# Kernel optimization log

Hardware: AMD Instinct MI355X
Metric: run time of the kernel (lower is better)

Reference implementation:

```python
import jax, jax.numpy as jnp
import numpy as np

N, L, C = 2, 1024, 256
H, E, CL, LAYERS = 64, 16, 64, 4


def setup_inputs() -> dict:
    key = jax.random.key(0)
    ks = jax.random.split(key, 12)
    s = 0.05
    return {
        "x": jax.random.normal(ks[0], (N, L, C), jnp.float32),
        "Wq": jax.random.normal(ks[1], (H * E, C), jnp.float32) * s,
        "bq": jax.random.normal(ks[2], (H * E,), jnp.float32) * s,
        "Wk": jax.random.normal(ks[3], (H * E, C), jnp.float32) * s,
        "bk": jax.random.normal(ks[4], (H * E,), jnp.float32) * s,
        "Wv": jax.random.normal(ks[5], (H, C), jnp.float32) * s,
        "bv": jax.random.normal(ks[6], (H,), jnp.float32) * s,
        "PE": jax.random.uniform(ks[7], (CL, H, E), jnp.float32),
        "fc_w": jax.random.normal(ks[8], (LAYERS, H, H), jnp.float32) * s,
        "fc_b": jax.random.normal(ks[9], (LAYERS, H), jnp.float32) * s,
        "Wout": jax.random.normal(ks[10], (3, H), jnp.float32) * s,
        "bout": jax.random.normal(ks[11], (3,), jnp.float32) * s,
    }


def reference(x, Wq, bq, Wk, bk, Wv, bv, PE, fc_w, fc_b, Wout, bout):
    n, l, c = x.shape
    cl, h, e_dim = PE.shape
    q = (x @ Wq.T + bq).reshape(n, l, h, e_dim)   # (N,L,H,E)
    k = (x @ Wk.T + bk).reshape(n, l, h, e_dim)   # (N,L,H,E)
    v = x @ Wv.T + bv                             # (N,L,H)
    # sliding-window offsets: row i gathers positions i..i+cl-1
    off = jnp.arange(l - cl)[:, None] + jnp.arange(cl)[None, :]  # (L-cl, cl)
    q_mid = q[:, cl // 2: l - cl // 2]            # (N,L-cl,H,E) center queries
    k_win = k[:, off]                             # (N,L-cl,cl,H,E) gathered keys
    # e_{h,id} = q.k + q.PE  (distributed instead of adding PE to k_win)
    e = (jnp.einsum('nlhe,nldhe->nldh', q_mid, k_win)
         + jnp.einsum('nlhe,dhe->nldh', q_mid, PE))
    a = jax.nn.softmax(e, axis=2)                 # softmax over window offset d
    v_win = v[:, off]                             # (N,L-cl,cl,H)
    out = jnp.einsum('nldh,nldh->nlh', a, v_win)  # weighted sum over d
    out = jax.nn.relu(out)
    for i in range(fc_w.shape[0]):                # 1x1 Conv1d stack == per-pos linear
        out = jax.nn.relu(jnp.einsum('nlh,oh->nlo', out, fc_w[i]) + fc_b[i])
    out = jnp.einsum('nlh,oh->nlo', out, Wout) + bout  # (N,L-cl,3)
    return out
```

## Files before the change

kernel.cpp:

```cpp
#include <hip/hip_runtime.h>


typedef __attribute__((ext_vector_type(8))) __bf16 bf16x8;
typedef __attribute__((ext_vector_type(8))) short short8;
typedef __attribute__((ext_vector_type(16))) float f32x16;

__device__ inline unsigned short bf16_rne(float x) {
    unsigned u = __builtin_bit_cast(unsigned, x);
    unsigned r = u + 0x7fffu + ((u >> 16) & 1u);
    return (unsigned short)(r >> 16);
}
__device__ inline float bf16_f(unsigned short h) {
    return __builtin_bit_cast(float, (unsigned)h << 16);
}

__global__ __launch_bounds__(256) void convert_split(
    const float* __restrict__ X,
    const float* __restrict__ Wq, const float* __restrict__ Wk, const float* __restrict__ Wv,
    unsigned short* __restrict__ XhG, unsigned short* __restrict__ XlG,
    unsigned short* __restrict__ WhG, unsigned short* __restrict__ WlG)
{
    const int g = blockIdx.x * 256 + threadIdx.x;
    const int NX = 131072;
    const int NW = 135168;
    if (g >= NX + NW) return;

    float4 v;
    unsigned short *dh, *dl;
    int off;
    if (g < NX) {
        off = g * 4;
        v = *reinterpret_cast<const float4*>(&X[off]);
        dh = XhG; dl = XlG;
    } else {
        off = (g - NX) * 4;
        const int row = off >> 8, col = off & 255;
        const float* s;
        if (row < 1024)      s = &Wq[row * 256 + col];
        else if (row < 2048) s = &Wk[(row - 1024) * 256 + col];
        else                 s = &Wv[(row - 2048) * 256 + col];
        v = *reinterpret_cast<const float4*>(s);
        dh = WhG; dl = WlG;
    }
    unsigned short h0 = bf16_rne(v.x), h1 = bf16_rne(v.y), h2 = bf16_rne(v.z), h3 = bf16_rne(v.w);
    unsigned short l0 = bf16_rne(v.x - bf16_f(h0));
    unsigned short l1 = bf16_rne(v.y - bf16_f(h1));
    unsigned short l2 = bf16_rne(v.z - bf16_f(h2));
    unsigned short l3 = bf16_rne(v.w - bf16_f(h3));
    ushort4 hv = make_ushort4(h0, h1, h2, h3);
    ushort4 lv = make_ushort4(l0, l1, l2, l3);
    *reinterpret_cast<ushort4*>(&dh[off]) = hv;
    *reinterpret_cast<ushort4*>(&dl[off]) = lv;
}

__device__ __forceinline__ bf16x8 ldsfrag2(const unsigned short* lds, int base, int row, int so) {
    return __builtin_bit_cast(bf16x8, *reinterpret_cast<const short8*>(
        lds + base + row * 64 + (((so ^ (row & 7)) & 7) << 3)));
}

__global__ __launch_bounds__(256, 3) void qkv_mfma(
    const unsigned short* __restrict__ XhG, const unsigned short* __restrict__ XlG,
    const unsigned short* __restrict__ WhG, const unsigned short* __restrict__ WlG,
    const float* __restrict__ bq, const float* __restrict__ bk, const float* __restrict__ bv,
    float* __restrict__ qT, float* __restrict__ kT, float* __restrict__ vT)
{
    __shared__ unsigned short lds[24576];

    const int tid  = threadIdx.x;
    const int lane = tid & 63;
    const int wid  = tid >> 6;
    const int wm   = wid >> 1;
    const int wn   = wid & 1;

    const int job = blockIdx.x;
    int m0, o0;
    if (job < 512) { m0 = (job & 31) * 64; o0 = (job >> 5) * 128; }
    else           { m0 = (job - 512) * 64; o0 = 2048; }

    f32x16 acc[2];
    #pragma unroll
    for (int j = 0; j < 2; ++j)
        acc[j] = f32x16{0.f,0.f,0.f,0.f,0.f,0.f,0.f,0.f,0.f,0.f,0.f,0.f,0.f,0.f,0.f,0.f};

    const int r8 = lane >> 3;
    const int ss = (lane & 7) ^ r8;

    const int arow = wm * 32 + (lane & 31);
    const int kh   = lane >> 5;

    for (int k0 = 0; k0 < 256; k0 += 64) {
        #pragma unroll
        for (int j = 0; j < 12; ++j) {
            const int c = wid * 12 + j;
            const unsigned short* gsrc;
            if (c < 8)       gsrc = &XhG[(m0 + (c << 3) + r8) * 256 + k0 + (ss << 3)];
            else if (c < 16) gsrc = &XlG[(m0 + ((c - 8) << 3) + r8) * 256 + k0 + (ss << 3)];
            else if (c < 32) gsrc = &WhG[(o0 + ((c - 16) << 3) + r8) * 256 + k0 + (ss << 3)];
            else             gsrc = &WlG[(o0 + ((c - 32) << 3) + r8) * 256 + k0 + (ss << 3)];
            char* lbase = (char*)lds + (c << 10);
            __builtin_amdgcn_global_load_lds(
                (const __attribute__((address_space(1))) void*)gsrc,
                (__attribute__((address_space(3))) void*)lbase, 16, 0, 0);
        }
        __syncthreads();

        #pragma unroll
        for (int kk = 0; kk < 64; kk += 16) {
            const int so = (kk >> 3) + kh;
            bf16x8 aH = ldsfrag2(lds, 0,     arow, so);
            bf16x8 aL = ldsfrag2(lds, 4096,  arow, so);
            #pragma unroll
            for (int ot = 0; ot < 2; ++ot) {
                const int brow = wn * 64 + ot * 32 + (lane & 31);
                bf16x8 bH = ldsfrag2(lds, 8192,  brow, so);
                bf16x8 bL = ldsfrag2(lds, 16384, brow, so);
                acc[ot] = __builtin_amdgcn_mfma_f32_32x32x16_bf16(aH, bH, acc[ot], 0, 0, 0);
                acc[ot] = __builtin_amdgcn_mfma_f32_32x32x16_bf16(aH, bL, acc[ot], 0, 0, 0);
                acc[ot] = __builtin_amdgcn_mfma_f32_32x32x16_bf16(aL, bH, acc[ot], 0, 0, 0);
            }
        }
        __syncthreads();
    }

    const int dcol = lane & 31;
    const int rbase4 = 4 * (lane >> 5);
    const int mode = (o0 < 1024) ? 0 : (o0 < 2048 ? 1 : 2);

    if (mode < 2) {
        float* __restrict__ T = mode ? kT : qT;
        const float* __restrict__ bias = mode ? bk : bq;
        const int ob = mode * 1024;
        #pragma unroll
        for (int ot = 0; ot < 2; ++ot) {
            const int o = o0 + wn * 64 + ot * 32 + dcol;
            const int h = (o >> 4) & 63;
            const int e = o & 15;
            const float bval = bias[o - ob];
            #pragma unroll
            for (int r = 0; r < 16; ++r) {
                const int mrow = (r & 3) + 8 * (r >> 2) + rbase4;
                const int m = m0 + wm * 32 + mrow;
                const int n = m >> 10, l = m & 1023;
                T[((n * 64 + h) * 1024 + l) * 16 + e] = acc[ot][r] + bval;
            }
        }
    } else if (wn == 0) {
        #pragma unroll
        for (int ot = 0; ot < 2; ++ot) {
            const int hV = ot * 32 + dcol;
            const float bval = bv[hV];
            #pragma unroll
            for (int r = 0; r < 16; ++r) {
                const int mrow = (r & 3) + 8 * (r >> 2) + rbase4;
                const int m = m0 + wm * 32 + mrow;
                const int n = m >> 10, l = m & 1023;
                vT[(n * 64 + hV) * 1024 + l] = acc[ot][r] + bval;
            }
        }
    }
}

__global__ __launch_bounds__(256) void attn_kernel(
    const float* __restrict__ qT, const float* __restrict__ kT,
    const float* __restrict__ vT, const float* __restrict__ PE,
    float* __restrict__ attT)
{
    __shared__ float2 kc[8 * 322];
    __shared__ float pe_lds[64 * 16];
    __shared__ float v_lds[320];

    const int tid  = threadIdx.x;
    const int lane = tid & 63;
    const int w    = tid >> 6;
    const int xb = blockIdx.x;
    const int h  = blockIdx.y;
    const int n  = blockIdx.z;
    const int l0 = xb * 256;

    const int nrows = min(319, 1024 - l0);
    const float4* kb4 = reinterpret_cast<const float4*>(kT + ((size_t)(n * 64 + h) * 1024 + l0) * 16);
    for (int u = tid; u < nrows * 4; u += 256) {
        const int row = u >> 2, f = u & 3;
        const float4 g = kb4[u];
        kc[(2 * f + 0) * 322 + row] = make_float2(g.x, g.y);
        kc[(2 * f + 1) * 322 + row] = make_float2(g.z, g.w);
    }
    {
        const int d = tid >> 2, f = tid & 3;
        *reinterpret_cast<float4*>(&pe_lds[d * 16 + f * 4]) =
            *reinterpret_cast<const float4*>(&PE[(d * 64 + h) * 16 + f * 4]);
    }
    const float* vbase = vT + (size_t)(n * 64 + h) * 1024 + l0;
    for (int u = tid; u < nrows; u += 256) v_lds[u] = vbase[u];

    const int lout = l0 + w * 64 + lane;
    const bool active = lout < 960;
    const int lq = active ? lout : 959;
    float4 q0, q1, q2, q3;
    {
        const float4* qb = reinterpret_cast<const float4*>(
            qT + ((size_t)(n * 64 + h) * 1024 + lq + 32) * 16);
        q0 = qb[0]; q1 = qb[1]; q2 = qb[2]; q3 = qb[3];
    }
    __syncthreads();

    const int rbase = w * 64 + lane;
    float den = 0.f, pv = 0.f;
    #pragma unroll 2
    for (int d = 0; d < 64; ++d) {
        const int r = rbase + d;
        const float2 c0 = kc[0 * 322 + r], c1 = kc[1 * 322 + r];
        const float2 c2 = kc[2 * 322 + r], c3 = kc[3 * 322 + r];
        const float2 c4 = kc[4 * 322 + r], c5 = kc[5 * 322 + r];
        const float2 c6 = kc[6 * 322 + r], c7 = kc[7 * 322 + r];
        const float4* pr = reinterpret_cast<const float4*>(&pe_lds[d * 16]);
        const float4 p0 = pr[0], p1 = pr[1], p2 = pr[2], p3 = pr[3];
        float s0 = (c0.x + p0.x) * q0.x + (c0.y + p0.y) * q0.y
                 + (c1.x + p0.z) * q0.z + (c1.y + p0.w) * q0.w;
        float s1 = (c2.x + p1.x) * q1.x + (c2.y + p1.y) * q1.y
                 + (c3.x + p1.z) * q1.z + (c3.y + p1.w) * q1.w;
        float s2 = (c4.x + p2.x) * q2.x + (c4.y + p2.y) * q2.y
                 + (c5.x + p2.z) * q2.z + (c5.y + p2.w) * q2.w;
        float s3 = (c6.x + p3.x) * q3.x + (c6.y + p3.y) * q3.y
                 + (c7.x + p3.z) * q3.z + (c7.y + p3.w) * q3.w;
        const float s = (s0 + s1) + (s2 + s3);
        const float p = __expf(s - 16.f);
        den += p;
        pv += p * v_lds[r];
    }
    if (active)
        attT[(size_t)(n * 64 + h) * 960 + lout] = fmaxf(pv / den, 0.f);
}

__global__ __launch_bounds__(512) void fc_kernel(
    const float* __restrict__ attT,
    const float* __restrict__ fc_w, const float* __restrict__ fc_b,
    const float* __restrict__ Wout, const float* __restrict__ bout,
    float* __restrict__ out)
{
    __shared__ float w_lds[64 * 68];
    __shared__ float wo_lds[3 * 64];
    __shared__ float bufA[16 * 68];
    __shared__ float bufB[16 * 68];

    const int tid = threadIdx.x;
    const int o  = tid & 63;
    const int rr = tid >> 6;
    const int blk = blockIdx.x;
    const int n  = blk / 60;
    const int l0 = (blk - n * 60) * 16;
    const int R0 = n * 960 + l0;

    for (int idx = tid; idx < 192; idx += 512) wo_lds[idx] = Wout[idx];
    for (int idx = tid; idx < 1024; idx += 512) {
        const int hh = idx >> 4, r = idx & 15;
        bufA[r * 68 + hh] = attT[(size_t)(n * 64 + hh) * 960 + l0 + r];
    }

    float* cur = bufA;
    float* nxt = bufB;

    for (int layer = 0; layer < 4; ++layer) {
        __syncthreads();
        const float4* wsrc = reinterpret_cast<const float4*>(fc_w + layer * 4096);
        for (int u = tid; u < 1024; u += 512) {
            const int oo = u >> 4, f = u & 15;
            *reinterpret_cast<float4*>(&w_lds[oo * 68 + f * 4]) = wsrc[u];
        }
        __syncthreads();
        const float bias = fc_b[layer * 64 + o];
        const float4* wr = reinterpret_cast<const float4*>(&w_lds[o * 68]);
        #pragma unroll
        for (int rb = 0; rb < 2; ++rb) {
            const int r = rr + rb * 8;
            float acc = bias;
            const float4* cr = reinterpret_cast<const float4*>(&cur[r * 68]);
            #pragma unroll
            for (int t = 0; t < 16; ++t) {
                const float4 c = cr[t], wv = wr[t];
                acc += c.x * wv.x + c.y * wv.y + c.z * wv.z + c.w * wv.w;
            }
            nxt[r * 68 + o] = fmaxf(acc, 0.f);
        }
        float* tmp = cur; cur = nxt; nxt = tmp;
    }
    __syncthreads();

    if (o < 3) {
        #pragma unroll
        for (int rb = 0; rb < 2; ++rb) {
            const int r = rr + rb * 8;
            float acc = bout[o];
            #pragma unroll
            for (int hh = 0; hh < 64; ++hh)
                acc += cur[r * 68 + hh] * wo_lds[o * 64 + hh];
            out[(R0 + r) * 3 + o] = acc;
        }
    }
}

extern "C" void kernel_launch(void* const* d_in, const int* in_sizes, int n_in,
                              void* d_out, int out_size, void* d_ws, size_t ws_size,
                              hipStream_t stream) {
    const float* x    = (const float*)d_in[0];
    const float* Wq   = (const float*)d_in[1];
    const float* bq   = (const float*)d_in[2];
    const float* Wk   = (const float*)d_in[3];
    const float* bk   = (const float*)d_in[4];
    const float* Wv   = (const float*)d_in[5];
    const float* bv   = (const float*)d_in[6];
    const float* PE   = (const float*)d_in[7];
    const float* fc_w = (const float*)d_in[8];
    const float* fc_b = (const float*)d_in[9];
    const float* Wout = (const float*)d_in[10];
    const float* bout = (const float*)d_in[11];
    float* out = (float*)d_out;

    float* ws = (float*)d_ws;
    float* qT   = ws;
    float* kT   = qT + 2097152;
    float* vT   = kT + 2097152;
    float* attT = vT + 131072;
    unsigned short* XhG = (unsigned short*)(attT + 122880);
    unsigned short* XlG = XhG + 524288;
    unsigned short* WhG = XlG + 524288;
    unsigned short* WlG = WhG + 540672;

    convert_split<<<1040, 256, 0, stream>>>(x, Wq, Wk, Wv, XhG, XlG, WhG, WlG);
    qkv_mfma<<<544, 256, 0, stream>>>(XhG, XlG, WhG, WlG, bq, bk, bv, qT, kT, vT);
    attn_kernel<<<dim3(4, 64, 2), 256, 0, stream>>>(qT, kT, vT, PE, attT);
    fc_kernel<<<120, 512, 0, stream>>>(attT, fc_w, fc_b, Wout, bout, out);
}
```

Baseline: 54.74 us.

## Fuse bf16 hi/lo split into QKV GEMM tile loads, drop convert kernel

Removes the separate convert_split kernel and its bf16 workspace. The QKV MFMA kernel now loads fp32 X and W directly into registers, splits each value into bf16 high and low parts, and writes them swizzled into LDS. This saves one launch and the round trip of the converted arrays through global memory. The trailing barrier was also dropped and the global loads were moved ahead of the first barrier, so the next tile's loads can overlap the previous MFMA work. In exchange, each block redoes the conversion for its own tiles (each element is converted once per block that loads it), and the direct global_load_lds path is replaced by register staging.

```diff
diff --git a/kernel.cpp b/kernel.cpp
--- a/kernel.cpp
+++ b/kernel.cpp
@@ -14,53 +14,14 @@
     return __builtin_bit_cast(float, (unsigned)h << 16);
 }
 
-__global__ __launch_bounds__(256) void convert_split(
-    const float* __restrict__ X,
-    const float* __restrict__ Wq, const float* __restrict__ Wk, const float* __restrict__ Wv,
-    unsigned short* __restrict__ XhG, unsigned short* __restrict__ XlG,
-    unsigned short* __restrict__ WhG, unsigned short* __restrict__ WlG)
-{
-    const int g = blockIdx.x * 256 + threadIdx.x;
-    const int NX = 131072;
-    const int NW = 135168;
-    if (g >= NX + NW) return;
-
-    float4 v;
-    unsigned short *dh, *dl;
-    int off;
-    if (g < NX) {
-        off = g * 4;
-        v = *reinterpret_cast<const float4*>(&X[off]);
-        dh = XhG; dl = XlG;
-    } else {
-        off = (g - NX) * 4;
-        const int row = off >> 8, col = off & 255;
-        const float* s;
-        if (row < 1024)      s = &Wq[row * 256 + col];
-        else if (row < 2048) s = &Wk[(row - 1024) * 256 + col];
-        else                 s = &Wv[(row - 2048) * 256 + col];
-        v = *reinterpret_cast<const float4*>(s);
-        dh = WhG; dl = WlG;
-    }
-    unsigned short h0 = bf16_rne(v.x), h1 = bf16_rne(v.y), h2 = bf16_rne(v.z), h3 = bf16_rne(v.w);
-    unsigned short l0 = bf16_rne(v.x - bf16_f(h0));
-    unsigned short l1 = bf16_rne(v.y - bf16_f(h1));
-    unsigned short l2 = bf16_rne(v.z - bf16_f(h2));
-    unsigned short l3 = bf16_rne(v.w - bf16_f(h3));
-    ushort4 hv = make_ushort4(h0, h1, h2, h3);
-    ushort4 lv = make_ushort4(l0, l1, l2, l3);
-    *reinterpret_cast<ushort4*>(&dh[off]) = hv;
-    *reinterpret_cast<ushort4*>(&dl[off]) = lv;
-}
-
 __device__ __forceinline__ bf16x8 ldsfrag2(const unsigned short* lds, int base, int row, int so) {
     return __builtin_bit_cast(bf16x8, *reinterpret_cast<const short8*>(
         lds + base + row * 64 + (((so ^ (row & 7)) & 7) << 3)));
 }
 
 __global__ __launch_bounds__(256, 3) void qkv_mfma(
-    const unsigned short* __restrict__ XhG, const unsigned short* __restrict__ XlG,
-    const unsigned short* __restrict__ WhG, const unsigned short* __restrict__ WlG,
+    const float* __restrict__ Xf,
+    const float* __restrict__ Wq, const float* __restrict__ Wk, const float* __restrict__ Wv,
     const float* __restrict__ bq, const float* __restrict__ bk, const float* __restrict__ bv,
     float* __restrict__ qT, float* __restrict__ kT, float* __restrict__ vT)
 {
@@ -82,25 +43,58 @@
     for (int j = 0; j < 2; ++j)
         acc[j] = f32x16{0.f,0.f,0.f,0.f,0.f,0.f,0.f,0.f,0.f,0.f,0.f,0.f,0.f,0.f,0.f,0.f};
 
-    const int r8 = lane >> 3;
-    const int ss = (lane & 7) ^ r8;
+    const int ra = tid >> 2, ca = (tid & 3) << 4;
+    const int rb = tid >> 1, cb = (tid & 1) << 5;
+    const float* arow_p = Xf + (m0 + ra) * 256;
+    const int orow = o0 + rb;
+    const float* brow_p;
+    if (orow < 1024)      brow_p = Wq + orow * 256;
+    else if (orow < 2048) brow_p = Wk + (orow - 1024) * 256;
+    else                  brow_p = Wv + (min(orow, 2111) - 2048) * 256;
 
     const int arow = wm * 32 + (lane & 31);
     const int kh   = lane >> 5;
 
     for (int k0 = 0; k0 < 256; k0 += 64) {
-        #pragma unroll
-        for (int j = 0; j < 12; ++j) {
-            const int c = wid * 12 + j;
-            const unsigned short* gsrc;
-            if (c < 8)       gsrc = &XhG[(m0 + (c << 3) + r8) * 256 + k0 + (ss << 3)];
-            else if (c < 16) gsrc = &XlG[(m0 + ((c - 8) << 3) + r8) * 256 + k0 + (ss << 3)];
-            else if (c < 32) gsrc = &WhG[(o0 + ((c - 16) << 3) + r8) * 256 + k0 + (ss << 3)];
-            else             gsrc = &WlG[(o0 + ((c - 32) << 3) + r8) * 256 + k0 + (ss << 3)];
-            char* lbase = (char*)lds + (c << 10);
-            __builtin_amdgcn_global_load_lds(
-                (const __attribute__((address_space(1))) void*)gsrc,
-                (__attribute__((address_space(3))) void*)lbase, 16, 0, 0);
+        float fa[16], fb[32];
+        #pragma unroll
+        for (int i = 0; i < 4; ++i)
+            *reinterpret_cast<float4*>(&fa[i * 4]) =
+                *reinterpret_cast<const float4*>(arow_p + k0 + ca + i * 4);
+        #pragma unroll
+        for (int i = 0; i < 8; ++i)
+            *reinterpret_cast<float4*>(&fb[i * 4]) =
+                *reinterpret_cast<const float4*>(brow_p + k0 + cb + i * 4);
+
+        __syncthreads();
+
+        #pragma unroll
+        for (int s2 = 0; s2 < 2; ++s2) {
+            short8 h8, l8;
+            #pragma unroll
+            for (int j = 0; j < 8; ++j) {
+                const float f = fa[s2 * 8 + j];
+                const unsigned short hh = bf16_rne(f);
+                h8[j] = (short)hh;
+                l8[j] = (short)bf16_rne(f - bf16_f(hh));
+            }
+            const int sp = ((((ca >> 3) + s2) ^ (ra & 7)) & 7) << 3;
+            *reinterpret_cast<short8*>(&lds[0    + ra * 64 + sp]) = h8;
+            *reinterpret_cast<short8*>(&lds[4096 + ra * 64 + sp]) = l8;
+        }
+        #pragma unroll
+        for (int s2 = 0; s2 < 4; ++s2) {
+            short8 h8, l8;
+            #pragma unroll
+            for (int j = 0; j < 8; ++j) {
+                const float f = fb[s2 * 8 + j];
+                const unsigned short hh = bf16_rne(f);
+                h8[j] = (short)hh;
+                l8[j] = (short)bf16_rne(f - bf16_f(hh));
+            }
+            const int sp = ((((cb >> 3) + s2) ^ (rb & 7)) & 7) << 3;
+            *reinterpret_cast<short8*>(&lds[8192  + rb * 64 + sp]) = h8;
+            *reinterpret_cast<short8*>(&lds[16384 + rb * 64 + sp]) = l8;
         }
         __syncthreads();
 
@@ -119,7 +113,6 @@
                 acc[ot] = __builtin_amdgcn_mfma_f32_32x32x16_bf16(aL, bH, acc[ot], 0, 0, 0);
             }
         }
-        __syncthreads();
     }
 
     const int dcol = lane & 31;
@@ -321,13 +314,8 @@
     float* kT   = qT + 2097152;
     float* vT   = kT + 2097152;
     float* attT = vT + 131072;
-    unsigned short* XhG = (unsigned short*)(attT + 122880);
-    unsigned short* XlG = XhG + 524288;
-    unsigned short* WhG = XlG + 524288;
-    unsigned short* WlG = WhG + 540672;
-
-    convert_split<<<1040, 256, 0, stream>>>(x, Wq, Wk, Wv, XhG, XlG, WhG, WlG);
-    qkv_mfma<<<544, 256, 0, stream>>>(XhG, XlG, WhG, WlG, bq, bk, bv, qT, kT, vT);
+
+    qkv_mfma<<<544, 256, 0, stream>>>(x, Wq, Wk, Wv, bq, bk, bv, qT, kT, vT);
     attn_kernel<<<dim3(4, 64, 2), 256, 0, stream>>>(qT, kT, vT, PE, attT);
     fc_kernel<<<120, 512, 0, stream>>>(attT, fc_w, fc_b, Wout, bout, out);
 }
```

New measurement: 57.01 us. 4.2% more time.
